# Kernel optimization log

Measured on AMD Instinct MI355X. Metric: run time of the kernel, lower is better.

## Reference

```python
import jax, jax.numpy as jnp
import numpy as np

INPUT_SIZE = 1000
EMB = 1024          # 2**ceil(log2(input_size))
NQ = 10             # log2(EMB)
NL = 3              # n_qlayers (hardcoded in module)
B = 4096


def _rot(phi, theta, omega):
    # PennyLane qml.Rot(phi, theta, omega) = RZ(omega) RY(theta) RZ(phi)
    c = jnp.cos(theta * 0.5).astype(jnp.complex64)
    s = jnp.sin(theta * 0.5).astype(jnp.complex64)
    ea = jnp.exp(-0.5j * (phi + omega))   # e^{-i(phi+omega)/2}
    eb = jnp.exp(0.5j * (phi - omega))    # e^{ i(phi-omega)/2}
    row0 = jnp.stack([ea * c, -eb * s])
    row1 = jnp.stack([jnp.conj(eb) * s, jnp.conj(ea) * c])
    return jnp.stack([row0, row1])        # [2, 2] complex64


def _apply_1q(psi, U, q):
    # psi: [B] + [2]*NQ ; contract qubit axis q+1 with U
    psi = jnp.tensordot(psi, U, axes=[[q + 1], [1]])
    return jnp.moveaxis(psi, -1, q + 1)


def _apply_cnot(psi, c, t):
    c_ax, t_ax = c + 1, t + 1
    psi0 = jax.lax.index_in_dim(psi, 0, axis=c_ax, keepdims=False)
    psi1 = jax.lax.index_in_dim(psi, 1, axis=c_ax, keepdims=False)
    f_ax = t_ax - 1 if t_ax > c_ax else t_ax
    psi1 = jnp.flip(psi1, axis=f_ax)      # X on target when control=1
    return jnp.stack([psi0, psi1], axis=c_ax)


def _circuit(x, w):
    # AmplitudeEmbedding(normalize=True) + StronglyEntanglingLayers + probs
    norm = jnp.sqrt(jnp.sum(x * x, axis=1, keepdims=True))
    psi = (x / norm).astype(jnp.complex64)
    b = psi.shape[0]
    psi = psi.reshape((b,) + (2,) * NQ)   # wire 0 = most-significant bit
    for l in range(NL):
        for q in range(NQ):
            psi = _apply_1q(psi, _rot(w[l, q, 0], w[l, q, 1], w[l, q, 2]), q)
        r = l % (NQ - 1) + 1              # default SEL ranges
        for q in range(NQ):
            psi = _apply_cnot(psi, q, (q + r) % NQ)
    return (psi.real ** 2 + psi.imag ** 2).reshape(b, -1)  # probs [B, 2**NQ]


def setup_inputs() -> dict:
    key = jax.random.key(0)
    ks = jax.random.split(key, 12)
    d = {
        'inputs': jax.random.normal(ks[0], (B, INPUT_SIZE), jnp.float32),
        'weightsEnc': 0.1 * jax.random.normal(ks[1], (NL, NQ, 3), jnp.float32),
        'weightsDec': 0.1 * jax.random.normal(ks[2], (NL, NQ, 3), jnp.float32),
        'W0': jax.random.normal(ks[3], (INPUT_SIZE, EMB), jnp.float32) / np.sqrt(INPUT_SIZE),
        'b0': jnp.zeros((EMB,), jnp.float32),
        'W1': jax.random.normal(ks[4], (EMB, 2 * EMB), jnp.float32) / np.sqrt(EMB),
        'b1': jnp.zeros((2 * EMB,), jnp.float32),
        'W2': jax.random.normal(ks[5], (2 * EMB, EMB), jnp.float32) / np.sqrt(2 * EMB),
        'b2': jnp.zeros((EMB,), jnp.float32),
        'W3': jax.random.normal(ks[6], (EMB, INPUT_SIZE), jnp.float32) / np.sqrt(EMB),
        'b3': jnp.zeros((INPUT_SIZE,), jnp.float32),
    }
    return d


def reference(inputs, weightsEnc, weightsDec, W0, b0, W1, b1, W2, b2, W3, b3):
    x = inputs @ W0 + b0                 # Dense(embedding_dim)
    x = _circuit(x, weightsEnc)          # encoder qnode (vmapped over batch)
    x = x @ W1 + b1                      # Dense(2*embedding_dim)
    x = x @ W2 + b2                      # Dense(embedding_dim)
    x = _circuit(x, weightsDec)          # decoder qnode
    x = x @ W3 + b3                      # Dense(input_size)
    x = jnp.abs(x)
    return x / jnp.sum(x, axis=1, keepdims=True)
```

## Files before the change

### kernel.cpp

```cpp
#include <hip/hip_runtime.h>
#include <math.h>


#define B_SZ 4096
#define EMB 1024
#define NQ 10
#define NL 3

typedef __bf16 bf16x8 __attribute__((ext_vector_type(8)));
typedef float f32x4 __attribute__((ext_vector_type(4)));
typedef unsigned short u16x8 __attribute__((ext_vector_type(8)));

__device__ __forceinline__ unsigned short f2bf_rne(float f) {
    unsigned int u = __float_as_uint(f);
    u += 0x7FFFu + ((u >> 16) & 1u);
    return (unsigned short)(u >> 16);
}
__device__ __forceinline__ float bf2f(unsigned short h) {
    return __uint_as_float(((unsigned int)h) << 16);
}
__device__ __forceinline__ float lane_bcast(float v, int l) {
    return __uint_as_float(__builtin_amdgcn_readlane(__float_as_uint(v), l));
}

template<int M>
__device__ __forceinline__ float lane_xor(float v) {
    if constexpr (M == 1)
        return __uint_as_float(__builtin_amdgcn_mov_dpp(__float_as_uint(v), 0xB1, 0xF, 0xF, true));
    else if constexpr (M == 2)
        return __uint_as_float(__builtin_amdgcn_mov_dpp(__float_as_uint(v), 0x4E, 0xF, 0xF, true));
    else if constexpr (M == 8)
        return __uint_as_float(__builtin_amdgcn_mov_dpp(__float_as_uint(v), 0x128, 0xF, 0xF, true));
    else if constexpr (M == 4)
        return __uint_as_float(__builtin_amdgcn_ds_swizzle(__float_as_uint(v), 0x101F));
    else if constexpr (M == 16)
        return __uint_as_float(__builtin_amdgcn_ds_swizzle(__float_as_uint(v), 0x401F));
    else
        return __shfl_xor(v, 32, 64);
}

__device__ __forceinline__ void gll16(const void* g, void* l) {
    __builtin_amdgcn_global_load_lds(
        (const __attribute__((address_space(1))) void*)g,
        (__attribute__((address_space(3))) void*)l, 16, 0, 0);
}

#define WAITCNT_VM(N) __builtin_amdgcn_s_waitcnt(0x0F70 | (N))

#define GBM 128
#define GBN 128
#define GBK 32

__global__ __launch_bounds__(512) void gemm3_mfma(
    const unsigned short* __restrict__ Ah, const unsigned short* __restrict__ Al,
    const unsigned short* __restrict__ Bh, const unsigned short* __restrict__ Bl,
    const float* __restrict__ bias, float* __restrict__ C,
    int Kp, int Np, int Ksplit, size_t zStride)
{
    __shared__ __align__(16) char lds[65536];

    const int tid = threadIdx.x;
    const int lane = tid & 63;
    const int wv = tid >> 6;
    const int wm = wv >> 1;
    const int wn = wv & 1;
    const int blockRow = blockIdx.y * GBM;
    const int blockCol = blockIdx.x * GBN;
    const int z = blockIdx.z;

    const int srow = tid >> 2;
    const int skel = (tid & 3) * 8;
    const size_t aOff = ((size_t)(blockRow + srow) * Kp + skel + (size_t)z * Ksplit) * 2;
    const size_t bOff = ((size_t)(blockCol + srow) * Kp + skel + (size_t)z * Ksplit) * 2;
    const char* aHp = (const char*)Ah + aOff;
    const char* aLp = (const char*)Al + aOff;
    const char* bHp = (const char*)Bh + bOff;
    const char* bLp = (const char*)Bl + bOff;
    const int stageOff = wv * 1024;

    f32x4 acc[2][4];
    #pragma unroll
    for (int i = 0; i < 2; ++i)
        #pragma unroll
        for (int j = 0; j < 4; ++j)
            #pragma unroll
            for (int r = 0; r < 4; ++r) acc[i][j][r] = 0.f;

    const int kq = (lane >> 4) * 16;
    int aFragOff[2], bFragOff[4];
    #pragma unroll
    for (int i = 0; i < 2; ++i) aFragOff[i] = (wm * 32 + i * 16 + (lane & 15)) * 64 + kq;
    #pragma unroll
    for (int j = 0; j < 4; ++j) bFragOff[j] = (wn * 64 + j * 16 + (lane & 15)) * 64 + kq;

    auto stage = [&](int s, int buf) {
        char* base = lds + buf * 32768;
        const size_t kb = (size_t)s * GBK * 2;
        gll16(aHp + kb, base + stageOff);
        gll16(aLp + kb, base + 8192 + stageOff);
        gll16(bHp + kb, base + 16384 + stageOff);
        gll16(bLp + kb, base + 24576 + stageOff);
    };

    const int nsteps = Ksplit / GBK;
    stage(0, 0);
    for (int s = 0; s < nsteps; ++s) {
        const int buf = s & 1;
        if (s + 1 < nsteps) {
            stage(s + 1, buf ^ 1);
            WAITCNT_VM(4);
        } else {
            WAITCNT_VM(0);
        }
        __builtin_amdgcn_s_barrier();

        char* base = lds + buf * 32768;
        bf16x8 ah[2], al[2], bh[4], bl[4];
        #pragma unroll
        for (int i = 0; i < 2; ++i) {
            ah[i] = *(const bf16x8*)(base + aFragOff[i]);
            al[i] = *(const bf16x8*)(base + 8192 + aFragOff[i]);
        }
        #pragma unroll
        for (int j = 0; j < 4; ++j) {
            bh[j] = *(const bf16x8*)(base + 16384 + bFragOff[j]);
            bl[j] = *(const bf16x8*)(base + 24576 + bFragOff[j]);
        }
        #pragma unroll
        for (int j = 0; j < 4; ++j)
            #pragma unroll
            for (int i = 0; i < 2; ++i) {
                acc[i][j] = __builtin_amdgcn_mfma_f32_16x16x32_bf16(al[i], bh[j], acc[i][j], 0, 0, 0);
                acc[i][j] = __builtin_amdgcn_mfma_f32_16x16x32_bf16(ah[i], bl[j], acc[i][j], 0, 0, 0);
                acc[i][j] = __builtin_amdgcn_mfma_f32_16x16x32_bf16(ah[i], bh[j], acc[i][j], 0, 0, 0);
            }
        __syncthreads();
    }

    float* Cz = C + (size_t)z * zStride;
    const bool addB = (z == 0) && (bias != nullptr);
    const int rquad = (lane >> 4) * 4;
    const int cidx = lane & 15;
    #pragma unroll
    for (int i = 0; i < 2; ++i)
        #pragma unroll
        for (int j = 0; j < 4; ++j) {
            #pragma unroll
            for (int r = 0; r < 4; ++r) {
                int row = blockRow + wm * 32 + i * 16 + rquad + r;
                int col = blockCol + wn * 64 + j * 16 + cidx;
                float v = acc[i][j][r];
                if (addB) v += bias[col];
                Cz[(size_t)row * Np + col] = v;
            }
        }
}

__device__ __forceinline__ void tsplit_block(
    const float* __restrict__ W, unsigned short* __restrict__ H, unsigned short* __restrict__ L,
    int K, int N, int Kp, int bx, int by, int tid)
{
    __shared__ float tile[32][33];
    const int tx = tid & 31, ty = tid >> 5;
    const int k0 = bx * 32, n0 = by * 32;
    #pragma unroll
    for (int i = 0; i < 4; ++i) {
        int k = k0 + ty + i * 8, n = n0 + tx;
        tile[ty + i * 8][tx] = (k < K && n < N) ? W[(size_t)k * N + n] : 0.f;
    }
    __syncthreads();
    #pragma unroll
    for (int i = 0; i < 4; ++i) {
        int n = n0 + ty + i * 8, k = k0 + tx;
        float v = tile[tx][ty + i * 8];
        size_t o = (size_t)n * Kp + k;
        unsigned short h = f2bf_rne(v);
        H[o] = h;
        L[o] = f2bf_rne(v - bf2f(h));
    }
}

__global__ __launch_bounds__(256) void prep_all_kernel(
    const float* __restrict__ W0, unsigned short* __restrict__ Bt0h, unsigned short* __restrict__ Bt0l,
    const float* __restrict__ W2, unsigned short* __restrict__ Bt2h, unsigned short* __restrict__ Bt2l,
    const float* __restrict__ W3, unsigned short* __restrict__ Bt3h, unsigned short* __restrict__ Bt3l,
    const float* __restrict__ W1, unsigned short* __restrict__ W1h, unsigned short* __restrict__ W1l,
    const float* __restrict__ X, unsigned short* __restrict__ Ah, unsigned short* __restrict__ Al,
    const float* __restrict__ b1, const float* __restrict__ b2, float* __restrict__ b12,
    const float* __restrict__ b3, float* __restrict__ b3p,
    const float* __restrict__ wEnc, const float* __restrict__ wDec, float* __restrict__ G)
{
    const int bid = blockIdx.x;
    const int tid = threadIdx.x;
    if (bid < 1024) {
        tsplit_block(W0, Bt0h, Bt0l, 1000, 1024, 1024, bid & 31, bid >> 5, tid);
    } else if (bid < 3072) {
        int b = bid - 1024;
        tsplit_block(W2, Bt2h, Bt2l, 2048, 1024, 2048, b & 63, b >> 6, tid);
    } else if (bid < 4096) {
        int b = bid - 3072;
        tsplit_block(W3, Bt3h, Bt3l, 1024, 1000, 1024, b & 31, b >> 5, tid);
    } else if (bid < 5120) {
        int r = bid - 4096;
        for (int c = tid; c < 2048; c += 256) {
            float v = W1[(size_t)r * 2048 + c];
            unsigned short h = f2bf_rne(v);
            size_t o = (size_t)r * 2048 + c;
            W1h[o] = h;
            W1l[o] = f2bf_rne(v - bf2f(h));
        }
    } else if (bid < 9216) {
        int r = bid - 5120;
        for (int c = tid; c < 1024; c += 256) {
            float v = (c < 1000) ? X[(size_t)r * 1000 + c] : 0.f;
            unsigned short h = f2bf_rne(v);
            size_t o = (size_t)r * 1024 + c;
            Ah[o] = h;
            Al[o] = f2bf_rne(v - bf2f(h));
        }
    } else if (bid < 9232) {
        __shared__ float red[4][64];
        const int tx = tid & 63, ty = tid >> 6;
        const int n = (bid - 9216) * 64 + tx;
        float s = 0.f;
        for (int j = ty * 512; j < (ty + 1) * 512; ++j)
            s += b1[j] * W2[(size_t)j * 1024 + n];
        red[ty][tx] = s;
        __syncthreads();
        if (ty == 0) b12[n] = red[0][tx] + red[1][tx] + red[2][tx] + red[3][tx] + b2[n];
    } else if (bid < 9236) {
        int i = (bid - 9232) * 256 + tid;
        b3p[i] = (i < 1000) ? b3[i] : 0.f;
    } else {
        int g = tid;
        if (g < 60) {
            const float* w = (g < 30) ? (wEnc + g * 3) : (wDec + (g - 30) * 3);
            float* o = G + ((g < 30) ? g : (g - 30 + 64)) * 8;
            float phi = w[0], th = w[1], om = w[2];
            float ch = cosf(0.5f * th), sh = sinf(0.5f * th);
            float ap = 0.5f * (phi + om), am = 0.5f * (phi - om);
            float cap = cosf(ap), sap = sinf(ap);
            float cam = cosf(am), sam = sinf(am);
            o[0] =  cap * ch; o[1] = -sap * ch;
            o[2] = -cam * sh; o[3] = -sam * sh;
            o[4] =  cam * sh; o[5] = -sam * sh;
            o[6] =  cap * ch; o[7] =  sap * ch;
        }
    }
}

__global__ __launch_bounds__(256) void tsplit8_kernel(
    const float* __restrict__ P, unsigned short* __restrict__ H, unsigned short* __restrict__ L)
{
    __shared__ float tile[32][33];
    const int tid = threadIdx.x;
    const int tx = tid & 31, ty = tid >> 5;
    const int k0 = blockIdx.x * 32, n0 = blockIdx.y * 32;
    #pragma unroll
    for (int i = 0; i < 4; ++i) {
        int k = k0 + ty + i * 8, n = n0 + tx;
        size_t o = (size_t)k * 1024 + n;
        float s = 0.f;
        #pragma unroll
        for (int zz = 0; zz < 8; ++zz) s += P[o + ((size_t)zz << 20)];
        tile[ty + i * 8][tx] = s;
    }
    __syncthreads();
    #pragma unroll
    for (int i = 0; i < 4; ++i) {
        int n = n0 + ty + i * 8, k = k0 + tx;
        float v = tile[tx][ty + i * 8];
        size_t o = (size_t)n * 1024 + k;
        unsigned short h = f2bf_rne(v);
        H[o] = h;
        L[o] = f2bf_rne(v - bf2f(h));
    }
}

template<int GATE, int Q>
__device__ __forceinline__ void apply_rot(float (&xr)[16], float (&xi)[16],
                                          const float (&tbl)[8], int lane)
{
    float are = lane_bcast(tbl[0], GATE), aim = lane_bcast(tbl[1], GATE);
    float bre = lane_bcast(tbl[2], GATE), bim = lane_bcast(tbl[3], GATE);
    float cre = lane_bcast(tbl[4], GATE), cim = lane_bcast(tbl[5], GATE);
    float dre = lane_bcast(tbl[6], GATE), dim_ = lane_bcast(tbl[7], GATE);
    constexpr int S = 1 << (9 - Q);
    if constexpr (S < 16) {
        #pragma unroll
        for (int p = 0; p < 8; ++p) {
            int r0 = (p / S) * (2 * S) + (p % S);
            int r1 = r0 + S;
            float x0r = xr[r0], x0i = xi[r0], x1r = xr[r1], x1i = xi[r1];
            xr[r0] = are * x0r - aim * x0i + bre * x1r - bim * x1i;
            xi[r0] = are * x0i + aim * x0r + bre * x1i + bim * x1r;
            xr[r1] = cre * x0r - cim * x0i + dre * x1r - dim_ * x1i;
            xi[r1] = cre * x0i + cim * x0r + dre * x1i + dim_ * x1r;
        }
    } else {
        constexpr int M = S >> 4;
        bool bit = (lane & M) != 0;
        float pre = bit ? dre : are, pim = bit ? dim_ : aim;
        float qre = bit ? cre : bre, qim = bit ? cim : bim;
        #pragma unroll
        for (int r = 0; r < 16; ++r) {
            float ore = lane_xor<M>(xr[r]);
            float oim = lane_xor<M>(xi[r]);
            float nr = pre * xr[r] - pim * xi[r] + qre * ore - qim * oim;
            float ni = pre * xi[r] + pim * xr[r] + qre * oim + qim * ore;
            xr[r] = nr; xi[r] = ni;
        }
    }
}

template<int C, int T>
__device__ __forceinline__ void apply_cnot(float (&xr)[16], float (&xi)[16], int lane)
{
    constexpr int SC = 1 << (9 - C), ST = 1 << (9 - T);
    if constexpr (SC < 16 && ST < 16) {
        #pragma unroll
        for (int r = 0; r < 16; ++r) {
            if ((r & SC) && !(r & ST)) {
                int j = r | ST;
                float t;
                t = xr[r]; xr[r] = xr[j]; xr[j] = t;
                t = xi[r]; xi[r] = xi[j]; xi[j] = t;
            }
        }
    } else if constexpr (SC < 16) {
        constexpr int MT = ST >> 4;
        #pragma unroll
        for (int r = 0; r < 16; ++r) {
            if (r & SC) {
                xr[r] = lane_xor<MT>(xr[r]);
                xi[r] = lane_xor<MT>(xi[r]);
            }
        }
    } else if constexpr (ST < 16) {
        constexpr int MC = SC >> 4;
        bool bit = (lane & MC) != 0;
        #pragma unroll
        for (int r = 0; r < 16; ++r) {
            if (!(r & ST)) {
                int j = r | ST;
                float a0 = xr[r], a1 = xr[j];
                xr[r] = bit ? a1 : a0;  xr[j] = bit ? a0 : a1;
                float b0 = xi[r], b1 = xi[j];
                xi[r] = bit ? b1 : b0;  xi[j] = bit ? b0 : b1;
            }
        }
    } else {
        constexpr int MC = SC >> 4, MT = ST >> 4;
        bool bit = (lane & MC) != 0;
        #pragma unroll
        for (int r = 0; r < 16; ++r) {
            float o = lane_xor<MT>(xr[r]);
            xr[r] = bit ? o : xr[r];
            float oi = lane_xor<MT>(xi[r]);
            xi[r] = bit ? oi : xi[r];
        }
    }
}

template<int L, int Q>
__device__ __forceinline__ void rots(float (&xr)[16], float (&xi)[16],
                                     const float (&tbl)[8], int lane) {
    apply_rot<L * 10 + Q, Q>(xr, xi, tbl, lane);
    if constexpr (Q < 9) rots<L, Q + 1>(xr, xi, tbl, lane);
}
template<int L, int Q>
__device__ __forceinline__ void cnots(float (&xr)[16], float (&xi)[16], int lane) {
    constexpr int R = (L % 9) + 1;
    apply_cnot<Q, (Q + R) % 10>(xr, xi, lane);
    if constexpr (Q < 9) cnots<L, Q + 1>(xr, xi, lane);
}

__global__ __launch_bounds__(256, 4) void circuit_reg_kernel(
    const float* __restrict__ X0, const float* __restrict__ X1,
    unsigned short* __restrict__ Ph, unsigned short* __restrict__ Pl,
    const float* __restrict__ G)
{
    const int lane = threadIdx.x & 63;
    const int item = blockIdx.x * 4 + (threadIdx.x >> 6);
    const size_t base = (size_t)item * 1024 + lane * 16;

    float tbl[8];
    {
        const float4* gp = (const float4*)(G + lane * 8);
        float4 t0 = gp[0], t1 = gp[1];
        tbl[0] = t0.x; tbl[1] = t0.y; tbl[2] = t0.z; tbl[3] = t0.w;
        tbl[4] = t1.x; tbl[5] = t1.y; tbl[6] = t1.z; tbl[7] = t1.w;
    }

    float xr[16], xi[16];
    const float4* xb0 = (const float4*)(X0 + base);
    const float4* xb1 = (const float4*)(X1 + base);
    #pragma unroll
    for (int v = 0; v < 4; ++v) {
        float4 f = xb0[v], g = xb1[v];
        xr[v * 4 + 0] = f.x + g.x; xr[v * 4 + 1] = f.y + g.y;
        xr[v * 4 + 2] = f.z + g.z; xr[v * 4 + 3] = f.w + g.w;
    }
    #pragma unroll
    for (int r = 0; r < 16; ++r) xi[r] = 0.f;

    float nrm = 0.f;
    #pragma unroll
    for (int r = 0; r < 16; ++r) nrm += xr[r] * xr[r];
    nrm += lane_xor<1>(nrm);
    nrm += lane_xor<2>(nrm);
    nrm += lane_xor<4>(nrm);
    nrm += lane_xor<8>(nrm);
    nrm += lane_xor<16>(nrm);
    nrm += lane_xor<32>(nrm);
    float inv = 1.0f / sqrtf(nrm);
    #pragma unroll
    for (int r = 0; r < 16; ++r) xr[r] *= inv;

    rots<0, 0>(xr, xi, tbl, lane);  cnots<0, 0>(xr, xi, lane);
    rots<1, 0>(xr, xi, tbl, lane);  cnots<1, 0>(xr, xi, lane);
    rots<2, 0>(xr, xi, tbl, lane);  cnots<2, 0>(xr, xi, lane);

    u16x8 h[2], lo[2];
    #pragma unroll
    for (int r = 0; r < 16; ++r) {
        float p = xr[r] * xr[r] + xi[r] * xi[r];
        unsigned short hh = f2bf_rne(p);
        h[r >> 3][r & 7] = hh;
        lo[r >> 3][r & 7] = f2bf_rne(p - bf2f(hh));
    }
    *(u16x8*)(Ph + base) = h[0];
    *(u16x8*)(Ph + base + 8) = h[1];
    *(u16x8*)(Pl + base) = lo[0];
    *(u16x8*)(Pl + base + 8) = lo[1];
}

__global__ __launch_bounds__(256) void absnorm_kernel(
    const float* __restrict__ P, size_t ZS, float* __restrict__ out, int N)
{
    __shared__ float red[4];
    const int row = blockIdx.x;
    const int tid = threadIdx.x;
    const size_t rb = (size_t)row * 1024 + tid * 4;

    float4 a = *(const float4*)(P + rb);
    float4 b = *(const float4*)(P + ZS + rb);
    float x[4] = { a.x + b.x, a.y + b.y, a.z + b.z, a.w + b.w };

    const int c0 = tid * 4;
    float s = 0.f;
    #pragma unroll
    for (int j = 0; j < 4; ++j) if (c0 + j < N) s += fabsf(x[j]);
    #pragma unroll
    for (int off = 32; off > 0; off >>= 1) s += __shfl_down(s, off);
    if ((tid & 63) == 0) red[tid >> 6] = s;
    __syncthreads();
    float inv = 1.0f / (red[0] + red[1] + red[2] + red[3]);
    #pragma unroll
    for (int j = 0; j < 4; ++j)
        if (c0 + j < N) out[(size_t)row * N + c0 + j] = fabsf(x[j]) * inv;
}

extern "C" void kernel_launch(void* const* d_in, const int* in_sizes, int n_in,
                              void* d_out, int out_size, void* d_ws, size_t ws_size,
                              hipStream_t stream)
{
    const float* inputs = (const float*)d_in[0];
    const float* wEnc   = (const float*)d_in[1];
    const float* wDec   = (const float*)d_in[2];
    const float* W0     = (const float*)d_in[3];
    const float* b0     = (const float*)d_in[4];
    const float* W1     = (const float*)d_in[5];
    const float* b1     = (const float*)d_in[6];
    const float* W2     = (const float*)d_in[7];
    const float* b2     = (const float*)d_in[8];
    const float* W3     = (const float*)d_in[9];
    const float* b3     = (const float*)d_in[10];
    float* out = (float*)d_out;

    char* w = (char*)d_ws;
    auto alloc = [&](size_t bytes) { char* p = w; w += (bytes + 255) & ~(size_t)255; return p; };

    unsigned short* Bt0h  = (unsigned short*)alloc((size_t)1024 * 1024 * 2);
    unsigned short* Bt0l  = (unsigned short*)alloc((size_t)1024 * 1024 * 2);
    unsigned short* Bt2h  = (unsigned short*)alloc((size_t)1024 * 2048 * 2);
    unsigned short* Bt2l  = (unsigned short*)alloc((size_t)1024 * 2048 * 2);
    unsigned short* Bt3h  = (unsigned short*)alloc((size_t)1024 * 1024 * 2);
    unsigned short* Bt3l  = (unsigned short*)alloc((size_t)1024 * 1024 * 2);
    unsigned short* Bt12h = (unsigned short*)alloc((size_t)1024 * 1024 * 2);
    unsigned short* Bt12l = (unsigned short*)alloc((size_t)1024 * 1024 * 2);
    unsigned short* W1h   = (unsigned short*)alloc((size_t)1024 * 2048 * 2);
    unsigned short* W1l   = (unsigned short*)alloc((size_t)1024 * 2048 * 2);
    float*          b3p   = (float*)alloc(1024 * 4);
    float*          b12   = (float*)alloc(1024 * 4);
    float*          G     = (float*)alloc(2 * 512 * 4);
    unsigned short* Ah    = (unsigned short*)alloc((size_t)B_SZ * 1024 * 2);
    unsigned short* Al    = (unsigned short*)alloc((size_t)B_SZ * 1024 * 2);
    unsigned short* ph    = (unsigned short*)alloc((size_t)B_SZ * 1024 * 2);
    unsigned short* pl    = (unsigned short*)alloc((size_t)B_SZ * 1024 * 2);
    float*          P     = (float*)alloc((size_t)2 * B_SZ * 1024 * 4);
    float* P12 = P;
    const size_t ZS = (size_t)B_SZ * 1024;

    dim3 blk256(256);

    prep_all_kernel<<<9237, blk256, 0, stream>>>(
        W0, Bt0h, Bt0l, W2, Bt2h, Bt2l, W3, Bt3h, Bt3l, W1, W1h, W1l,
        inputs, Ah, Al, b1, b2, b12, b3, b3p, wEnc, wDec, G);

    gemm3_mfma<<<dim3(8, 8, 8), 512, 0, stream>>>(
        W1h, W1l, Bt2h, Bt2l, nullptr, P12, 2048, 1024, 256, (size_t)1 << 20);
    tsplit8_kernel<<<dim3(32, 32), blk256, 0, stream>>>(P12, Bt12h, Bt12l);

    gemm3_mfma<<<dim3(8, 32, 2), 512, 0, stream>>>(
        Ah, Al, Bt0h, Bt0l, b0, P, 1024, 1024, 512, ZS);
    circuit_reg_kernel<<<B_SZ / 4, blk256, 0, stream>>>(P, P + ZS, ph, pl, G);
    gemm3_mfma<<<dim3(8, 32, 2), 512, 0, stream>>>(
        ph, pl, Bt12h, Bt12l, b12, P, 1024, 1024, 512, ZS);
    circuit_reg_kernel<<<B_SZ / 4, blk256, 0, stream>>>(P, P + ZS, ph, pl, G + 512);
    gemm3_mfma<<<dim3(8, 32, 2), 512, 0, stream>>>(
        ph, pl, Bt3h, Bt3l, b3p, P, 1024, 1024, 512, ZS);
    absnorm_kernel<<<B_SZ, blk256, 0, stream>>>(P, ZS, out, 1000);
}
```

Baseline: 407.6 us.

## Split each circuit state vector across two wavefronts with LDS exchange for top qubit

The quantum circuit kernel now assigns each 1024-amplitude state to two wavefronts of 512 amplitudes each, instead of one wavefront of 1024. Each lane holds 8 complex amplitudes in registers instead of 16, which cuts register pressure and allows higher occupancy (launch bounds raised to 6 blocks). Gates on the most-significant qubit, and CNOTs that involve it, now exchange data through shared memory with block-wide barriers. The norm reduction is also combined across the two halves through shared memory. The cost is extra barriers and LDS traffic in exchange for twice as many wavefronts, which gives more latency hiding.

```diff
diff --git a/kernel.cpp b/kernel.cpp
--- a/kernel.cpp
+++ b/kernel.cpp
@@ -277,18 +277,19 @@
     }
 }
 
+
 template<int GATE, int Q>
-__device__ __forceinline__ void apply_rot(float (&xr)[16], float (&xi)[16],
-                                          const float (&tbl)[8], int lane)
+__device__ __forceinline__ void apply_rot2(float (&xr)[8], float (&xi)[8],
+    const float (&tbl)[8], int lane, int half, float2 (&xc)[2][8][64])
 {
     float are = lane_bcast(tbl[0], GATE), aim = lane_bcast(tbl[1], GATE);
     float bre = lane_bcast(tbl[2], GATE), bim = lane_bcast(tbl[3], GATE);
     float cre = lane_bcast(tbl[4], GATE), cim = lane_bcast(tbl[5], GATE);
     float dre = lane_bcast(tbl[6], GATE), dim_ = lane_bcast(tbl[7], GATE);
     constexpr int S = 1 << (9 - Q);
-    if constexpr (S < 16) {
-        #pragma unroll
-        for (int p = 0; p < 8; ++p) {
+    if constexpr (S < 8) {
+        #pragma unroll
+        for (int p = 0; p < 4; ++p) {
             int r0 = (p / S) * (2 * S) + (p % S);
             int r1 = r0 + S;
             float x0r = xr[r0], x0i = xi[r0], x1r = xr[r1], x1i = xi[r1];
@@ -297,29 +298,92 @@
             xr[r1] = cre * x0r - cim * x0i + dre * x1r - dim_ * x1i;
             xi[r1] = cre * x0i + cim * x0r + dre * x1i + dim_ * x1r;
         }
-    } else {
-        constexpr int M = S >> 4;
+    } else if constexpr (S < 512) {
+        constexpr int M = S >> 3;
         bool bit = (lane & M) != 0;
         float pre = bit ? dre : are, pim = bit ? dim_ : aim;
         float qre = bit ? cre : bre, qim = bit ? cim : bim;
         #pragma unroll
-        for (int r = 0; r < 16; ++r) {
+        for (int r = 0; r < 8; ++r) {
             float ore = lane_xor<M>(xr[r]);
             float oim = lane_xor<M>(xi[r]);
             float nr = pre * xr[r] - pim * xi[r] + qre * ore - qim * oim;
             float ni = pre * xi[r] + pim * xr[r] + qre * oim + qim * ore;
             xr[r] = nr; xi[r] = ni;
         }
+    } else {
+        #pragma unroll
+        for (int r = 0; r < 8; ++r) xc[half][r][lane] = make_float2(xr[r], xi[r]);
+        __syncthreads();
+        float pre = half ? dre : are, pim = half ? dim_ : aim;
+        float qre = half ? cre : bre, qim = half ? cim : bim;
+        #pragma unroll
+        for (int r = 0; r < 8; ++r) {
+            float2 o = xc[half ^ 1][r][lane];
+            float nr = pre * xr[r] - pim * xi[r] + qre * o.x - qim * o.y;
+            float ni = pre * xi[r] + pim * xr[r] + qre * o.y + qim * o.x;
+            xr[r] = nr; xi[r] = ni;
+        }
+        __syncthreads();
     }
 }
 
 template<int C, int T>
-__device__ __forceinline__ void apply_cnot(float (&xr)[16], float (&xi)[16], int lane)
+__device__ __forceinline__ void apply_cnot2(float (&xr)[8], float (&xi)[8],
+    int lane, int half, float2 (&xc)[2][8][64])
 {
     constexpr int SC = 1 << (9 - C), ST = 1 << (9 - T);
-    if constexpr (SC < 16 && ST < 16) {
-        #pragma unroll
-        for (int r = 0; r < 16; ++r) {
+    if constexpr (SC >= 512) {
+        if (half) {
+            if constexpr (ST >= 8) {
+                constexpr int MT = ST >> 3;
+                #pragma unroll
+                for (int r = 0; r < 8; ++r) {
+                    xr[r] = lane_xor<MT>(xr[r]);
+                    xi[r] = lane_xor<MT>(xi[r]);
+                }
+            } else {
+                #pragma unroll
+                for (int r = 0; r < 8; ++r) {
+                    if (!(r & ST)) {
+                        int j = r | ST;
+                        float t;
+                        t = xr[r]; xr[r] = xr[j]; xr[j] = t;
+                        t = xi[r]; xi[r] = xi[j]; xi[j] = t;
+                    }
+                }
+            }
+        }
+    } else if constexpr (ST >= 512) {
+        if constexpr (SC < 8) {
+            #pragma unroll
+            for (int r = 0; r < 8; ++r)
+                if (r & SC) xc[half][r][lane] = make_float2(xr[r], xi[r]);
+            __syncthreads();
+            #pragma unroll
+            for (int r = 0; r < 8; ++r)
+                if (r & SC) {
+                    float2 o = xc[half ^ 1][r][lane];
+                    xr[r] = o.x; xi[r] = o.y;
+                }
+            __syncthreads();
+        } else {
+            constexpr int MC = SC >> 3;
+            #pragma unroll
+            for (int r = 0; r < 8; ++r) xc[half][r][lane] = make_float2(xr[r], xi[r]);
+            __syncthreads();
+            if (lane & MC) {
+                #pragma unroll
+                for (int r = 0; r < 8; ++r) {
+                    float2 o = xc[half ^ 1][r][lane];
+                    xr[r] = o.x; xi[r] = o.y;
+                }
+            }
+            __syncthreads();
+        }
+    } else if constexpr (SC < 8 && ST < 8) {
+        #pragma unroll
+        for (int r = 0; r < 8; ++r) {
             if ((r & SC) && !(r & ST)) {
                 int j = r | ST;
                 float t;
@@ -327,20 +391,20 @@
                 t = xi[r]; xi[r] = xi[j]; xi[j] = t;
             }
         }
-    } else if constexpr (SC < 16) {
-        constexpr int MT = ST >> 4;
-        #pragma unroll
-        for (int r = 0; r < 16; ++r) {
+    } else if constexpr (SC < 8) {
+        constexpr int MT = ST >> 3;
+        #pragma unroll
+        for (int r = 0; r < 8; ++r) {
             if (r & SC) {
                 xr[r] = lane_xor<MT>(xr[r]);
                 xi[r] = lane_xor<MT>(xi[r]);
             }
         }
-    } else if constexpr (ST < 16) {
-        constexpr int MC = SC >> 4;
+    } else if constexpr (ST < 8) {
+        constexpr int MC = SC >> 3;
         bool bit = (lane & MC) != 0;
         #pragma unroll
-        for (int r = 0; r < 16; ++r) {
+        for (int r = 0; r < 8; ++r) {
             if (!(r & ST)) {
                 int j = r | ST;
                 float a0 = xr[r], a1 = xr[j];
@@ -350,10 +414,10 @@
             }
         }
     } else {
-        constexpr int MC = SC >> 4, MT = ST >> 4;
+        constexpr int MC = SC >> 3, MT = ST >> 3;
         bool bit = (lane & MC) != 0;
         #pragma unroll
-        for (int r = 0; r < 16; ++r) {
+        for (int r = 0; r < 8; ++r) {
             float o = lane_xor<MT>(xr[r]);
             xr[r] = bit ? o : xr[r];
             float oi = lane_xor<MT>(xi[r]);
@@ -363,26 +427,33 @@
 }
 
 template<int L, int Q>
-__device__ __forceinline__ void rots(float (&xr)[16], float (&xi)[16],
-                                     const float (&tbl)[8], int lane) {
-    apply_rot<L * 10 + Q, Q>(xr, xi, tbl, lane);
-    if constexpr (Q < 9) rots<L, Q + 1>(xr, xi, tbl, lane);
+__device__ __forceinline__ void rots2(float (&xr)[8], float (&xi)[8],
+    const float (&tbl)[8], int lane, int half, float2 (&xc)[2][8][64]) {
+    apply_rot2<L * 10 + Q, Q>(xr, xi, tbl, lane, half, xc);
+    if constexpr (Q < 9) rots2<L, Q + 1>(xr, xi, tbl, lane, half, xc);
 }
 template<int L, int Q>
-__device__ __forceinline__ void cnots(float (&xr)[16], float (&xi)[16], int lane) {
+__device__ __forceinline__ void cnots2(float (&xr)[8], float (&xi)[8],
+    int lane, int half, float2 (&xc)[2][8][64]) {
     constexpr int R = (L % 9) + 1;
-    apply_cnot<Q, (Q + R) % 10>(xr, xi, lane);
-    if constexpr (Q < 9) cnots<L, Q + 1>(xr, xi, lane);
-}
-
-__global__ __launch_bounds__(256, 4) void circuit_reg_kernel(
+    apply_cnot2<Q, (Q + R) % 10>(xr, xi, lane, half, xc);
+    if constexpr (Q < 9) cnots2<L, Q + 1>(xr, xi, lane, half, xc);
+}
+
+__global__ __launch_bounds__(256, 6) void circuit2w_kernel(
     const float* __restrict__ X0, const float* __restrict__ X1,
     unsigned short* __restrict__ Ph, unsigned short* __restrict__ Pl,
     const float* __restrict__ G)
 {
+    __shared__ float2 xch[2][2][8][64];
+    __shared__ float nsum[2][2];
+
     const int lane = threadIdx.x & 63;
-    const int item = blockIdx.x * 4 + (threadIdx.x >> 6);
-    const size_t base = (size_t)item * 1024 + lane * 16;
+    const int wv = threadIdx.x >> 6;
+    const int it = wv >> 1;
+    const int half = wv & 1;
+    const int item = blockIdx.x * 2 + it;
+    const size_t base = (size_t)item * 1024 + (size_t)half * 512 + lane * 8;
 
     float tbl[8];
     {
@@ -392,47 +463,47 @@
         tbl[4] = t1.x; tbl[5] = t1.y; tbl[6] = t1.z; tbl[7] = t1.w;
     }
 
-    float xr[16], xi[16];
-    const float4* xb0 = (const float4*)(X0 + base);
-    const float4* xb1 = (const float4*)(X1 + base);
-    #pragma unroll
-    for (int v = 0; v < 4; ++v) {
-        float4 f = xb0[v], g = xb1[v];
+    float xr[8], xi[8];
+    const float4* a0 = (const float4*)(X0 + base);
+    const float4* a1 = (const float4*)(X1 + base);
+    #pragma unroll
+    for (int v = 0; v < 2; ++v) {
+        float4 f = a0[v], g = a1[v];
         xr[v * 4 + 0] = f.x + g.x; xr[v * 4 + 1] = f.y + g.y;
         xr[v * 4 + 2] = f.z + g.z; xr[v * 4 + 3] = f.w + g.w;
     }
     #pragma unroll
-    for (int r = 0; r < 16; ++r) xi[r] = 0.f;
-
-    float nrm = 0.f;
-    #pragma unroll
-    for (int r = 0; r < 16; ++r) nrm += xr[r] * xr[r];
-    nrm += lane_xor<1>(nrm);
-    nrm += lane_xor<2>(nrm);
-    nrm += lane_xor<4>(nrm);
-    nrm += lane_xor<8>(nrm);
-    nrm += lane_xor<16>(nrm);
-    nrm += lane_xor<32>(nrm);
-    float inv = 1.0f / sqrtf(nrm);
-    #pragma unroll
-    for (int r = 0; r < 16; ++r) xr[r] *= inv;
-
-    rots<0, 0>(xr, xi, tbl, lane);  cnots<0, 0>(xr, xi, lane);
-    rots<1, 0>(xr, xi, tbl, lane);  cnots<1, 0>(xr, xi, lane);
-    rots<2, 0>(xr, xi, tbl, lane);  cnots<2, 0>(xr, xi, lane);
-
-    u16x8 h[2], lo[2];
-    #pragma unroll
-    for (int r = 0; r < 16; ++r) {
+    for (int r = 0; r < 8; ++r) xi[r] = 0.f;
+
+    float s = 0.f;
+    #pragma unroll
+    for (int r = 0; r < 8; ++r) s += xr[r] * xr[r];
+    s += lane_xor<1>(s);
+    s += lane_xor<2>(s);
+    s += lane_xor<4>(s);
+    s += lane_xor<8>(s);
+    s += lane_xor<16>(s);
+    s += lane_xor<32>(s);
+    if (lane == 0) nsum[it][half] = s;
+    __syncthreads();
+    float inv = 1.0f / sqrtf(nsum[it][0] + nsum[it][1]);
+    #pragma unroll
+    for (int r = 0; r < 8; ++r) xr[r] *= inv;
+
+    rots2<0, 0>(xr, xi, tbl, lane, half, xch[it]);  cnots2<0, 0>(xr, xi, lane, half, xch[it]);
+    rots2<1, 0>(xr, xi, tbl, lane, half, xch[it]);  cnots2<1, 0>(xr, xi, lane, half, xch[it]);
+    rots2<2, 0>(xr, xi, tbl, lane, half, xch[it]);  cnots2<2, 0>(xr, xi, lane, half, xch[it]);
+
+    u16x8 h, lo;
+    #pragma unroll
+    for (int r = 0; r < 8; ++r) {
         float p = xr[r] * xr[r] + xi[r] * xi[r];
         unsigned short hh = f2bf_rne(p);
-        h[r >> 3][r & 7] = hh;
-        lo[r >> 3][r & 7] = f2bf_rne(p - bf2f(hh));
-    }
-    *(u16x8*)(Ph + base) = h[0];
-    *(u16x8*)(Ph + base + 8) = h[1];
-    *(u16x8*)(Pl + base) = lo[0];
-    *(u16x8*)(Pl + base + 8) = lo[1];
+        h[r] = hh;
+        lo[r] = f2bf_rne(p - bf2f(hh));
+    }
+    *(u16x8*)(Ph + base) = h;
+    *(u16x8*)(Pl + base) = lo;
 }
 
 __global__ __launch_bounds__(256) void absnorm_kernel(
@@ -514,10 +585,10 @@
 
     gemm3_mfma<<<dim3(8, 32, 2), 512, 0, stream>>>(
         Ah, Al, Bt0h, Bt0l, b0, P, 1024, 1024, 512, ZS);
-    circuit_reg_kernel<<<B_SZ / 4, blk256, 0, stream>>>(P, P + ZS, ph, pl, G);
+    circuit2w_kernel<<<2048, blk256, 0, stream>>>(P, P + ZS, ph, pl, G);
     gemm3_mfma<<<dim3(8, 32, 2), 512, 0, stream>>>(
         ph, pl, Bt12h, Bt12l, b12, P, 1024, 1024, 512, ZS);
-    circuit_reg_kernel<<<B_SZ / 4, blk256, 0, stream>>>(P, P + ZS, ph, pl, G + 512);
+    circuit2w_kernel<<<2048, blk256, 0, stream>>>(P, P + ZS, ph, pl, G + 512);
     gemm3_mfma<<<dim3(8, 32, 2), 512, 0, stream>>>(
         ph, pl, Bt3h, Bt3l, b3p, P, 1024, 1024, 512, ZS);
     absnorm_kernel<<<B_SZ, blk256, 0, stream>>>(P, ZS, out, 1000);
```

New measurement: 403.4 us. No clear change (-1.0%).

## Merge independent GEMMs and tsplit with circuit into dual-role launches

Applied to the files above, without the earlier changes.

The W1·W2 weight-product GEMM and the first activation GEMM now run in a single launch, with block indices split between the two problems. The transpose/split of their product is likewise fused into the same launch as the first circuit kernel. This removes two kernel launches and lets independent work fill the GPU together. P12 gets its own buffer so the two GEMMs no longer alias. Separately, the circuit layer loop is no longer unrolled and takes the gate index at runtime, which shrinks code size but adds runtime readlane indexing.

```diff
diff --git a/kernel.cpp b/kernel.cpp
--- a/kernel.cpp
+++ b/kernel.cpp
@@ -51,22 +51,20 @@
 #define GBN 128
 #define GBK 32
 
-__global__ __launch_bounds__(512) void gemm3_mfma(
+__device__ __forceinline__ void gemm_body(
     const unsigned short* __restrict__ Ah, const unsigned short* __restrict__ Al,
     const unsigned short* __restrict__ Bh, const unsigned short* __restrict__ Bl,
     const float* __restrict__ bias, float* __restrict__ C,
-    int Kp, int Np, int Ksplit, size_t zStride)
-{
-    __shared__ __align__(16) char lds[65536];
-
-    const int tid = threadIdx.x;
+    int Kp, int Np, int Ksplit, size_t zStride,
+    int bx, int by, int bz, int tid, char* lds)
+{
     const int lane = tid & 63;
     const int wv = tid >> 6;
     const int wm = wv >> 1;
     const int wn = wv & 1;
-    const int blockRow = blockIdx.y * GBM;
-    const int blockCol = blockIdx.x * GBN;
-    const int z = blockIdx.z;
+    const int blockRow = by * GBM;
+    const int blockCol = bx * GBN;
+    const int z = bz;
 
     const int srow = tid >> 2;
     const int skel = (tid & 3) * 8;
@@ -154,6 +152,37 @@
                 Cz[(size_t)row * Np + col] = v;
             }
         }
+}
+
+__global__ __launch_bounds__(512) void gemm3_mfma(
+    const unsigned short* __restrict__ Ah, const unsigned short* __restrict__ Al,
+    const unsigned short* __restrict__ Bh, const unsigned short* __restrict__ Bl,
+    const float* __restrict__ bias, float* __restrict__ C,
+    int Kp, int Np, int Ksplit, size_t zStride)
+{
+    __shared__ __align__(16) char lds[65536];
+    gemm_body(Ah, Al, Bh, Bl, bias, C, Kp, Np, Ksplit, zStride,
+              blockIdx.x, blockIdx.y, blockIdx.z, threadIdx.x, lds);
+}
+
+__global__ __launch_bounds__(512) void gemm_dual(
+    const unsigned short* __restrict__ A0h, const unsigned short* __restrict__ A0l,
+    const unsigned short* __restrict__ B0h, const unsigned short* __restrict__ B0l,
+    const float* __restrict__ bias0, float* __restrict__ C0,
+    const unsigned short* __restrict__ A1h, const unsigned short* __restrict__ A1l,
+    const unsigned short* __restrict__ B1h, const unsigned short* __restrict__ B1l,
+    float* __restrict__ C1)
+{
+    __shared__ __align__(16) char lds[65536];
+    const int b = blockIdx.x;
+    if (b < 512) {
+        gemm_body(A0h, A0l, B0h, B0l, bias0, C0, 1024, 1024, 512,
+                  (size_t)B_SZ * 1024, b & 7, (b >> 3) & 31, b >> 8, threadIdx.x, lds);
+    } else {
+        const int b1 = b - 512;
+        gemm_body(A1h, A1l, B1h, B1l, nullptr, C1, 2048, 1024, 256,
+                  (size_t)1 << 20, b1 & 7, (b1 >> 3) & 7, b1 >> 6, threadIdx.x, lds);
+    }
 }
 
 __device__ __forceinline__ void tsplit_block(
@@ -249,42 +278,15 @@
     }
 }
 
-__global__ __launch_bounds__(256) void tsplit8_kernel(
-    const float* __restrict__ P, unsigned short* __restrict__ H, unsigned short* __restrict__ L)
-{
-    __shared__ float tile[32][33];
-    const int tid = threadIdx.x;
-    const int tx = tid & 31, ty = tid >> 5;
-    const int k0 = blockIdx.x * 32, n0 = blockIdx.y * 32;
-    #pragma unroll
-    for (int i = 0; i < 4; ++i) {
-        int k = k0 + ty + i * 8, n = n0 + tx;
-        size_t o = (size_t)k * 1024 + n;
-        float s = 0.f;
-        #pragma unroll
-        for (int zz = 0; zz < 8; ++zz) s += P[o + ((size_t)zz << 20)];
-        tile[ty + i * 8][tx] = s;
-    }
-    __syncthreads();
-    #pragma unroll
-    for (int i = 0; i < 4; ++i) {
-        int n = n0 + ty + i * 8, k = k0 + tx;
-        float v = tile[tx][ty + i * 8];
-        size_t o = (size_t)n * 1024 + k;
-        unsigned short h = f2bf_rne(v);
-        H[o] = h;
-        L[o] = f2bf_rne(v - bf2f(h));
-    }
-}
-
-template<int GATE, int Q>
-__device__ __forceinline__ void apply_rot(float (&xr)[16], float (&xi)[16],
-                                          const float (&tbl)[8], int lane)
-{
-    float are = lane_bcast(tbl[0], GATE), aim = lane_bcast(tbl[1], GATE);
-    float bre = lane_bcast(tbl[2], GATE), bim = lane_bcast(tbl[3], GATE);
-    float cre = lane_bcast(tbl[4], GATE), cim = lane_bcast(tbl[5], GATE);
-    float dre = lane_bcast(tbl[6], GATE), dim_ = lane_bcast(tbl[7], GATE);
+
+template<int Q>
+__device__ __forceinline__ void apply_rot_d(float (&xr)[16], float (&xi)[16],
+                                            const float (&tbl)[8], int lane, int gate)
+{
+    float are = lane_bcast(tbl[0], gate), aim = lane_bcast(tbl[1], gate);
+    float bre = lane_bcast(tbl[2], gate), bim = lane_bcast(tbl[3], gate);
+    float cre = lane_bcast(tbl[4], gate), cim = lane_bcast(tbl[5], gate);
+    float dre = lane_bcast(tbl[6], gate), dim_ = lane_bcast(tbl[7], gate);
     constexpr int S = 1 << (9 - Q);
     if constexpr (S < 16) {
         #pragma unroll
@@ -313,6 +315,13 @@
     }
 }
 
+template<int Q>
+__device__ __forceinline__ void rots_d(float (&xr)[16], float (&xi)[16],
+                                       const float (&tbl)[8], int lane, int base) {
+    apply_rot_d<Q>(xr, xi, tbl, lane, base + Q);
+    if constexpr (Q < 9) rots_d<Q + 1>(xr, xi, tbl, lane, base);
+}
+
 template<int C, int T>
 __device__ __forceinline__ void apply_cnot(float (&xr)[16], float (&xi)[16], int lane)
 {
@@ -363,25 +372,17 @@
 }
 
 template<int L, int Q>
-__device__ __forceinline__ void rots(float (&xr)[16], float (&xi)[16],
-                                     const float (&tbl)[8], int lane) {
-    apply_rot<L * 10 + Q, Q>(xr, xi, tbl, lane);
-    if constexpr (Q < 9) rots<L, Q + 1>(xr, xi, tbl, lane);
-}
-template<int L, int Q>
 __device__ __forceinline__ void cnots(float (&xr)[16], float (&xi)[16], int lane) {
     constexpr int R = (L % 9) + 1;
     apply_cnot<Q, (Q + R) % 10>(xr, xi, lane);
     if constexpr (Q < 9) cnots<L, Q + 1>(xr, xi, lane);
 }
 
-__global__ __launch_bounds__(256, 4) void circuit_reg_kernel(
+__device__ __forceinline__ void circuit_body(
     const float* __restrict__ X0, const float* __restrict__ X1,
     unsigned short* __restrict__ Ph, unsigned short* __restrict__ Pl,
-    const float* __restrict__ G)
-{
-    const int lane = threadIdx.x & 63;
-    const int item = blockIdx.x * 4 + (threadIdx.x >> 6);
+    const float* __restrict__ G, int item, int lane)
+{
     const size_t base = (size_t)item * 1024 + lane * 16;
 
     float tbl[8];
@@ -417,9 +418,13 @@
     #pragma unroll
     for (int r = 0; r < 16; ++r) xr[r] *= inv;
 
-    rots<0, 0>(xr, xi, tbl, lane);  cnots<0, 0>(xr, xi, lane);
-    rots<1, 0>(xr, xi, tbl, lane);  cnots<1, 0>(xr, xi, lane);
-    rots<2, 0>(xr, xi, tbl, lane);  cnots<2, 0>(xr, xi, lane);
+    #pragma clang loop unroll(disable)
+    for (int l = 0; l < 3; ++l) {
+        rots_d<0>(xr, xi, tbl, lane, l * 10);
+        if (l == 0)      cnots<0, 0>(xr, xi, lane);
+        else if (l == 1) cnots<1, 0>(xr, xi, lane);
+        else             cnots<2, 0>(xr, xi, lane);
+    }
 
     u16x8 h[2], lo[2];
     #pragma unroll
@@ -433,6 +438,52 @@
     *(u16x8*)(Ph + base + 8) = h[1];
     *(u16x8*)(Pl + base) = lo[0];
     *(u16x8*)(Pl + base + 8) = lo[1];
+}
+
+__global__ __launch_bounds__(256, 4) void circuit_reg_kernel(
+    const float* __restrict__ X0, const float* __restrict__ X1,
+    unsigned short* __restrict__ Ph, unsigned short* __restrict__ Pl,
+    const float* __restrict__ G)
+{
+    circuit_body(X0, X1, Ph, Pl, G,
+                 blockIdx.x * 4 + (threadIdx.x >> 6), threadIdx.x & 63);
+}
+
+__global__ __launch_bounds__(256, 4) void fused_ts_circ_kernel(
+    const float* __restrict__ P12, unsigned short* __restrict__ H, unsigned short* __restrict__ L,
+    const float* __restrict__ X0, const float* __restrict__ X1,
+    unsigned short* __restrict__ Ph, unsigned short* __restrict__ Pl,
+    const float* __restrict__ G)
+{
+    __shared__ float tile[32][33];
+    const int bid = blockIdx.x;
+    const int tid = threadIdx.x;
+    if (bid < 1024) {
+        const int tx = tid & 31, ty = tid >> 5;
+        const int k0 = (bid & 31) * 32, n0 = (bid >> 5) * 32;
+        #pragma unroll
+        for (int i = 0; i < 4; ++i) {
+            int k = k0 + ty + i * 8, n = n0 + tx;
+            size_t o = (size_t)k * 1024 + n;
+            float s = 0.f;
+            #pragma unroll
+            for (int zz = 0; zz < 8; ++zz) s += P12[o + ((size_t)zz << 20)];
+            tile[ty + i * 8][tx] = s;
+        }
+        __syncthreads();
+        #pragma unroll
+        for (int i = 0; i < 4; ++i) {
+            int n = n0 + ty + i * 8, k = k0 + tx;
+            float v = tile[tx][ty + i * 8];
+            size_t o = (size_t)n * 1024 + k;
+            unsigned short h = f2bf_rne(v);
+            H[o] = h;
+            L[o] = f2bf_rne(v - bf2f(h));
+        }
+    } else {
+        circuit_body(X0, X1, Ph, Pl, G,
+                     (bid - 1024) * 4 + (tid >> 6), tid & 63);
+    }
 }
 
 __global__ __launch_bounds__(256) void absnorm_kernel(
@@ -499,7 +550,7 @@
     unsigned short* ph    = (unsigned short*)alloc((size_t)B_SZ * 1024 * 2);
     unsigned short* pl    = (unsigned short*)alloc((size_t)B_SZ * 1024 * 2);
     float*          P     = (float*)alloc((size_t)2 * B_SZ * 1024 * 4);
-    float* P12 = P;
+    float*          P12   = (float*)alloc((size_t)8 * 1024 * 1024 * 4);
     const size_t ZS = (size_t)B_SZ * 1024;
 
     dim3 blk256(256);
@@ -508,17 +559,20 @@
         W0, Bt0h, Bt0l, W2, Bt2h, Bt2l, W3, Bt3h, Bt3l, W1, W1h, W1l,
         inputs, Ah, Al, b1, b2, b12, b3, b3p, wEnc, wDec, G);
 
-    gemm3_mfma<<<dim3(8, 8, 8), 512, 0, stream>>>(
-        W1h, W1l, Bt2h, Bt2l, nullptr, P12, 2048, 1024, 256, (size_t)1 << 20);
-    tsplit8_kernel<<<dim3(32, 32), blk256, 0, stream>>>(P12, Bt12h, Bt12l);
-
-    gemm3_mfma<<<dim3(8, 32, 2), 512, 0, stream>>>(
-        Ah, Al, Bt0h, Bt0l, b0, P, 1024, 1024, 512, ZS);
-    circuit_reg_kernel<<<B_SZ / 4, blk256, 0, stream>>>(P, P + ZS, ph, pl, G);
+    gemm_dual<<<1024, 512, 0, stream>>>(
+        Ah, Al, Bt0h, Bt0l, b0, P,
+        W1h, W1l, Bt2h, Bt2l, P12);
+
+    fused_ts_circ_kernel<<<2048, blk256, 0, stream>>>(
+        P12, Bt12h, Bt12l, P, P + ZS, ph, pl, G);
+
     gemm3_mfma<<<dim3(8, 32, 2), 512, 0, stream>>>(
         ph, pl, Bt12h, Bt12l, b12, P, 1024, 1024, 512, ZS);
-    circuit_reg_kernel<<<B_SZ / 4, blk256, 0, stream>>>(P, P + ZS, ph, pl, G + 512);
+
+    circuit_reg_kernel<<<1024, blk256, 0, stream>>>(P, P + ZS, ph, pl, G + 512);
+
     gemm3_mfma<<<dim3(8, 32, 2), 512, 0, stream>>>(
         ph, pl, Bt3h, Bt3l, b3p, P, 1024, 1024, 512, ZS);
+
     absnorm_kernel<<<B_SZ, blk256, 0, stream>>>(P, ZS, out, 1000);
 }
```

Result: faster. 371.3 us (-8.9%).
